# Kernel optimization log

Measured on AMD Instinct MI355X. Metric: run time of the kernel, lower is better.

The kernel has to match this reference:

```python
import jax, jax.numpy as jnp
import numpy as np

MAX_DIST = 32
NUM_HEADS = 16


def setup_inputs() -> dict:
    key = jax.random.key(0)
    ks = jax.random.split(key, 10)
    D = 1024
    B, S = 2, 2048
    hd = D // NUM_HEADS
    sc = 0.02
    return {
        "x": jax.random.normal(ks[0], (B, S, D), dtype=jnp.float32),
        "Wq": jax.random.normal(ks[1], (D, D), dtype=jnp.float32) * sc,
        "bq": jax.random.normal(ks[2], (D,), dtype=jnp.float32) * sc,
        "Wk": jax.random.normal(ks[3], (D, D), dtype=jnp.float32) * sc,
        "bk": jax.random.normal(ks[4], (D,), dtype=jnp.float32) * sc,
        "Wv": jax.random.normal(ks[5], (D, D), dtype=jnp.float32) * sc,
        "bv": jax.random.normal(ks[6], (D,), dtype=jnp.float32) * sc,
        "Wo": jax.random.normal(ks[7], (D, D), dtype=jnp.float32) * sc,
        "bo": jax.random.normal(ks[8], (D,), dtype=jnp.float32) * sc,
        "rel_emb": jax.random.normal(ks[9], (2 * MAX_DIST + 1, hd), dtype=jnp.float32) * sc,
    }


def reference(x, Wq, bq, Wk, bk, Wv, bv, Wo, bo, rel_emb):
    B, S, D = x.shape
    H = NUM_HEADS
    hd = D // H
    scale = hd ** -0.5

    def proj(W, b):
        # [B,S,D] -> [B,H,S,hd]
        return (x @ W + b).reshape(B, S, H, hd).transpose(0, 2, 1, 3)

    q = proj(Wq, bq)
    k = proj(Wk, bk)
    v = proj(Wv, bv)

    # relative position embedding lookup: [S,S,hd]
    pos = jnp.arange(S)
    rel = jnp.clip(pos[:, None] - pos[None, :], -MAX_DIST, MAX_DIST) + MAX_DIST
    rpe = rel_emb[rel]  # [S,S,hd]

    cc = jnp.einsum('bhqd,bhkd->bhqk', q, k) * scale
    cp = jnp.einsum('bhqd,qkd->bhqk', q, rpe) * scale
    attn = jax.nn.softmax(cc + cp, axis=-1)
    ctx = jnp.einsum('bhqk,bhkd->bhqd', attn, v)  # [B,H,S,hd]
    ctx = ctx.transpose(0, 2, 1, 3).reshape(B, S, D)
    return ctx @ Wo + bo
```

## Files before the change

kernel.cpp:

```cpp
#include <hip/hip_runtime.h>

typedef __attribute__((ext_vector_type(4))) float f32x4;
typedef __attribute__((ext_vector_type(8))) short bf16x8;

#define SEQ    2048
#define HD     64
#define NBH    32
#define MTOK   4096
#define DMODEL 1024
#define QBLK   128

__device__ __forceinline__ unsigned short f2b(float f) {
  unsigned int u = __float_as_uint(f);
  u += 0x7fffu + ((u >> 16) & 1u);
  return (unsigned short)(u >> 16);
}
__device__ __forceinline__ float b2f(unsigned short s) {
  return __uint_as_float(((unsigned int)s) << 16);
}
__device__ __forceinline__ unsigned int cvtpk_bf16(float lo, float hi) {
  unsigned int r;
  asm("v_cvt_pk_bf16_f32 %0, %1, %2" : "=v"(r) : "v"(lo), "v"(hi));
  return r;
}
__device__ __forceinline__ void gload16(const void* g, void* l) {
  __builtin_amdgcn_global_load_lds(
      (const __attribute__((address_space(1))) unsigned int*)g,
      (__attribute__((address_space(3))) unsigned int*)l, 16, 0, 0);
}

__global__ __launch_bounds__(256) void k_convert_x(const float* __restrict__ x,
                                                   unsigned short* __restrict__ xb) {
  int i = blockIdx.x * 256 + threadIdx.x;
  float4 v = ((const float4*)x)[i];
  ushort4 o;
  o.x = f2b(v.x); o.y = f2b(v.y); o.z = f2b(v.z); o.w = f2b(v.w);
  ((ushort4*)xb)[i] = o;
}

__global__ __launch_bounds__(256) void k_wtrans(const float* __restrict__ W,
                                                unsigned short* __restrict__ Wt) {
  __shared__ float tile[64 * 65];
  int bi = blockIdx.x, bj = blockIdx.y, t = threadIdx.x;
  for (int p = 0; p < 16; p++) {
    int e = p * 256 + t;
    int r = e >> 6, c = e & 63;
    tile[r * 65 + c] = W[(size_t)(bi * 64 + r) * DMODEL + bj * 64 + c];
  }
  __syncthreads();
  for (int p = 0; p < 16; p++) {
    int e = p * 256 + t;
    int n = e >> 6, k = e & 63;
    Wt[(size_t)(bj * 64 + n) * DMODEL + bi * 64 + k] = f2b(tile[k * 65 + n]);
  }
}

template <int MODE>
__global__ __launch_bounds__(256) void k_gemm_bt(
    const unsigned short* __restrict__ A, const unsigned short* __restrict__ Bt,
    int M, int N, int K,
    const float* __restrict__ bias0, const float* __restrict__ bias1,
    const float* __restrict__ bias2,
    float* __restrict__ Cf,
    unsigned short* __restrict__ Qo, unsigned short* __restrict__ Ko,
    unsigned short* __restrict__ Vo) {
  __shared__ unsigned short As[128 * 64];
  __shared__ unsigned short Bs[128 * 64];
  int bm = blockIdx.x, bn = blockIdx.y;
  int tid = threadIdx.x;
  int w = tid >> 6, lane = tid & 63;
  int lg = lane >> 4, lc = lane & 15;
  int wm = (w >> 1) * 64, wn = (w & 1) * 64;
  f32x4 acc[4][4];
  for (int a = 0; a < 4; a++)
    for (int b = 0; b < 4; b++) acc[a][b] = (f32x4){0.f, 0.f, 0.f, 0.f};
  const unsigned short* ag = A + (size_t)(bm * 128) * K;
  const unsigned short* bg = Bt + (size_t)(bn * 128) * K;
  for (int k0 = 0; k0 < K; k0 += 64) {
    __syncthreads();
    for (int p = 0; p < 4; p++) {
      int c = (w * 4 + p) * 64 + lane;
      int r = c >> 3, ch = (c & 7) ^ (r & 7);
      gload16(ag + (size_t)r * K + k0 + ch * 8, &As[c * 8]);
      gload16(bg + (size_t)r * K + k0 + ch * 8, &Bs[c * 8]);
    }
    __syncthreads();
    for (int kk = 0; kk < 2; kk++) {
      bf16x8 av[4], bv[4];
      for (int mi = 0; mi < 4; mi++) {
        int row = wm + mi * 16 + lc;
        av[mi] = *(const bf16x8*)&As[row * 64 + ((kk * 32 + lg * 8) ^ ((row & 7) << 3))];
      }
      for (int ni = 0; ni < 4; ni++) {
        int row = wn + ni * 16 + lc;
        bv[ni] = *(const bf16x8*)&Bs[row * 64 + ((kk * 32 + lg * 8) ^ ((row & 7) << 3))];
      }
      for (int mi = 0; mi < 4; mi++)
        for (int ni = 0; ni < 4; ni++)
          acc[mi][ni] = __builtin_amdgcn_mfma_f32_16x16x32_bf16(av[mi], bv[ni], acc[mi][ni], 0, 0, 0);
    }
  }
  for (int mi = 0; mi < 4; mi++) {
    for (int i = 0; i < 4; i++) {
      int row = bm * 128 + wm + mi * 16 + 4 * lg + i;
      for (int ni = 0; ni < 4; ni++) {
        int col = bn * 128 + wn + ni * 16 + lc;
        float v = acc[mi][ni][i];
        if (MODE == 0) {
          Cf[(size_t)row * N + col] = v + bias0[col];
        } else {
          int which = col >> 10, hcol = col & 1023;
          const float* bb = which == 0 ? bias0 : (which == 1 ? bias1 : bias2);
          unsigned short* dst = which == 0 ? Qo : (which == 1 ? Ko : Vo);
          int b = row >> 11, s = row & 2047;
          int h = hcol >> 6, d = hcol & 63;
          dst[(((size_t)(b * 16 + h)) * SEQ + s) * HD + d] = f2b(v + bb[hcol]);
        }
      }
    }
  }
}

__global__ __launch_bounds__(256) void k_transpose_v(const unsigned short* __restrict__ V,
                                                     unsigned short* __restrict__ Vt) {
  __shared__ unsigned short tile[64 * 72];
  int sc = blockIdx.x, bh = blockIdx.y, t = threadIdx.x;
  int s0 = sc * 64;
  for (int p = 0; p < 16; p++) {
    int e = p * 256 + t;
    int r = e >> 6, c = e & 63;
    tile[r * 72 + c] = V[(((size_t)bh) * SEQ + s0 + r) * HD + c];
  }
  __syncthreads();
  for (int p = 0; p < 16; p++) {
    int e = p * 256 + t;
    int d = e >> 6, j = e & 63;
    Vt[(((size_t)bh) * HD + d) * SEQ + s0 + j] = tile[j * 72 + d];
  }
}

__global__ __launch_bounds__(256) void k_qr(const unsigned short* __restrict__ Qb,
                                            const float* __restrict__ rel_emb,
                                            float* __restrict__ qr) {
  __shared__ float relS[65 * 66];
  __shared__ unsigned short qS[32 * 64];
  int sc = blockIdx.x, bh = blockIdx.y, t = threadIdx.x;
  int s0 = sc * 32;
  for (int i = t; i < 65 * 64; i += 256) relS[(i >> 6) * 66 + (i & 63)] = rel_emb[i];
  for (int i = t; i < 32 * 64; i += 256) qS[i] = Qb[((size_t)bh * SEQ + s0) * HD + i];
  __syncthreads();
  for (int e = t; e < 32 * 65; e += 256) {
    int sl = e / 65, r = e % 65;
    float acc = 0.f;
    for (int d = 0; d < 64; d++) acc += b2f(qS[sl * 64 + d]) * relS[r * 66 + d];
    qr[((size_t)bh * SEQ + s0 + sl) * 65 + r] = acc;
  }
}

#define C1 0.180336880f
#define C2 11.5415603f
__global__ __launch_bounds__(512, 4) void k_attn(const unsigned short* __restrict__ Qb,
                                                 const unsigned short* __restrict__ Kb,
                                                 const unsigned short* __restrict__ Vtb,
                                                 const float* __restrict__ qr,
                                                 unsigned short* __restrict__ ctx) {
  __shared__ unsigned short Ks[64 * 64];
  __shared__ unsigned short Vts[64 * 64];
  __shared__ unsigned short Ps[8][16 * 64];
  __shared__ float qrs[QBLK * 65];
  int qt = blockIdx.x, bh = blockIdx.y;
  int tid = threadIdx.x, w = tid >> 6, lane = tid & 63;
  int lg = lane >> 4, lc = lane & 15;
  int q0 = qt * QBLK, qw = q0 + w * 16;

  {
    const float* src = qr + ((size_t)bh * SEQ + q0) * 65;
    for (int i = tid; i < QBLK * 65; i += 512) qrs[i] = src[i];
  }
  bf16x8 aq[2];
  {
    const unsigned short* qp = Qb + ((size_t)bh * SEQ + qw + lc) * HD + lg * 8;
    aq[0] = *(const bf16x8*)qp;
    aq[1] = *(const bf16x8*)(qp + 32);
  }
  f32x4 o[4];
  float l[4];
  for (int n = 0; n < 4; n++) o[n] = (f32x4){0.f, 0.f, 0.f, 0.f};
  for (int i = 0; i < 4; i++) l[i] = 0.f;
  __syncthreads();

  float blo[4], bhi[4];
  for (int i = 0; i < 4; i++) {
    int rl = w * 16 + 4 * lg + i;
    blo[i] = fmaf(qrs[rl * 65],      C1, -C2);
    bhi[i] = fmaf(qrs[rl * 65 + 64], C1, -C2);
  }

  for (int kt = 0; kt < SEQ / 64; kt++) {
    int k0 = kt * 64;
    const unsigned short* kg = Kb + ((size_t)bh * SEQ + k0) * HD;
    const unsigned short* vg = Vtb + ((size_t)bh * HD) * SEQ + k0;
    {
      int c = tid;
      int r = c >> 3, ch = (c & 7) ^ (r & 7);
      gload16(kg + (size_t)r * HD + ch * 8, &Ks[c * 8]);
      gload16(vg + (size_t)r * SEQ + ch * 8, &Vts[c * 8]);
    }
    __syncthreads();

    f32x4 s[4];
    #pragma unroll
    for (int n = 0; n < 4; n++) s[n] = (f32x4){0.f, 0.f, 0.f, 0.f};
    #pragma unroll
    for (int n = 0; n < 4; n++) {
      int row = n * 16 + lc;
      #pragma unroll
      for (int kk = 0; kk < 2; kk++) {
        bf16x8 bk = *(const bf16x8*)&Ks[row * 64 + ((kk * 32 + lg * 8) ^ ((row & 7) << 3))];
        s[n] = __builtin_amdgcn_mfma_f32_16x16x32_bf16(aq[kk], bk, s[n], 0, 0, 0);
      }
    }

    int dw = qw - k0;
    bool gather = (dw >= -32) && (dw <= 80);
    #pragma unroll
    for (int n = 0; n < 4; n++)
      #pragma unroll
      for (int i = 0; i < 4; i++) {
        float bf;
        if (gather) {
          int rl = w * 16 + 4 * lg + i;
          int rel = rl + q0 - k0 - n * 16 - lc;
          rel = rel < -32 ? -32 : (rel > 32 ? 32 : rel);
          bf = fmaf(qrs[rl * 65 + rel + 32], C1, -C2);
        } else {
          bf = (dw < 0) ? blo[i] : bhi[i];
        }
        float p = __builtin_amdgcn_exp2f(fmaf(s[n][i], C1, bf));
        s[n][i] = p;
        l[i] += p;
      }

    #pragma unroll
    for (int n = 0; n < 4; n++)
      #pragma unroll
      for (int i = 0; i < 4; i += 2) {
        unsigned int u = cvtpk_bf16(s[n][i], s[n][i + 1]);
        int r0 = 4 * lg + i, r1 = r0 + 1;
        Ps[w][r0 * 64 + ((n * 16 + lc) ^ ((r0 & 7) << 3))] = (unsigned short)u;
        Ps[w][r1 * 64 + ((n * 16 + lc) ^ ((r1 & 7) << 3))] = (unsigned short)(u >> 16);
      }

    #pragma unroll
    for (int kk = 0; kk < 2; kk++) {
      bf16x8 ap = *(const bf16x8*)&Ps[w][lc * 64 + ((kk * 32 + lg * 8) ^ ((lc & 7) << 3))];
      #pragma unroll
      for (int n = 0; n < 4; n++) {
        int row = n * 16 + lc;
        bf16x8 bv = *(const bf16x8*)&Vts[row * 64 + ((kk * 32 + lg * 8) ^ ((row & 7) << 3))];
        o[n] = __builtin_amdgcn_mfma_f32_16x16x32_bf16(ap, bv, o[n], 0, 0, 0);
      }
    }
    __syncthreads();
  }

  int b = bh >> 4, h = bh & 15;
  for (int i = 0; i < 4; i++) {
    float t = l[i];
    t += __shfl_xor(t, 1);
    t += __shfl_xor(t, 2);
    t += __shfl_xor(t, 4);
    t += __shfl_xor(t, 8);
    float inv = 1.f / t;
    int row = qw + 4 * lg + i;
    size_t base = ((size_t)(b * SEQ + row)) * DMODEL + h * HD;
    for (int n = 0; n < 4; n++) ctx[base + n * 16 + lc] = f2b(o[n][i] * inv);
  }
}

extern "C" void kernel_launch(void* const* d_in, const int* in_sizes, int n_in,
                              void* d_out, int out_size, void* d_ws, size_t ws_size,
                              hipStream_t stream) {
  const float* x   = (const float*)d_in[0];
  const float* Wq  = (const float*)d_in[1];
  const float* bq  = (const float*)d_in[2];
  const float* Wk  = (const float*)d_in[3];
  const float* bk  = (const float*)d_in[4];
  const float* Wv  = (const float*)d_in[5];
  const float* bv  = (const float*)d_in[6];
  const float* Wo  = (const float*)d_in[7];
  const float* bo  = (const float*)d_in[8];
  const float* rel = (const float*)d_in[9];
  float* out = (float*)d_out;

  char* ws = (char*)d_ws;
  size_t off = 0;
  auto carve = [&](size_t bytes) -> void* {
    void* p = ws + off;
    off += (bytes + 255) & ~(size_t)255;
    return p;
  };
  unsigned short* xb   = (unsigned short*)carve((size_t)MTOK * DMODEL * 2);
  unsigned short* Wqkv = (unsigned short*)carve((size_t)3 * DMODEL * DMODEL * 2);
  unsigned short* Wot  = (unsigned short*)carve((size_t)DMODEL * DMODEL * 2);
  unsigned short* Qb   = (unsigned short*)carve((size_t)NBH * SEQ * HD * 2);
  unsigned short* Kb   = (unsigned short*)carve((size_t)NBH * SEQ * HD * 2);
  unsigned short* Vb   = (unsigned short*)carve((size_t)NBH * SEQ * HD * 2);
  unsigned short* Vtb  = (unsigned short*)carve((size_t)NBH * SEQ * HD * 2);
  float*          qr   = (float*)carve((size_t)NBH * SEQ * 65 * 4);
  unsigned short* ctx  = (unsigned short*)carve((size_t)MTOK * DMODEL * 2);

  k_convert_x<<<MTOK * DMODEL / 4 / 256, 256, 0, stream>>>(x, xb);
  k_wtrans<<<dim3(16, 16), 256, 0, stream>>>(Wq, Wqkv);
  k_wtrans<<<dim3(16, 16), 256, 0, stream>>>(Wk, Wqkv + (size_t)DMODEL * DMODEL);
  k_wtrans<<<dim3(16, 16), 256, 0, stream>>>(Wv, Wqkv + (size_t)2 * DMODEL * DMODEL);
  k_wtrans<<<dim3(16, 16), 256, 0, stream>>>(Wo, Wot);
  k_gemm_bt<1><<<dim3(32, 24), 256, 0, stream>>>(xb, Wqkv, MTOK, 3 * DMODEL, DMODEL,
                                                 bq, bk, bv, nullptr, Qb, Kb, Vb);
  k_transpose_v<<<dim3(32, 32), 256, 0, stream>>>(Vb, Vtb);
  k_qr<<<dim3(64, 32), 256, 0, stream>>>(Qb, rel, qr);
  k_attn<<<dim3(SEQ / QBLK, NBH), 512, 0, stream>>>(Qb, Kb, Vtb, qr, ctx);
  k_gemm_bt<0><<<dim3(32, 8), 256, 0, stream>>>(ctx, Wot, MTOK, DMODEL, DMODEL,
                                                bo, nullptr, nullptr, out,
                                                nullptr, nullptr, nullptr);
}
```

Baseline: 184.1 us.

## Merge small prep kernels, reorder attention grid, add MFMA priority hints

Folds the four weight-transpose launches into one 3D-grid launch, and merges the V transpose and q·rel_emb kernels into one launch that branches on block index. The attention grid is swapped so consecutive blocks walk across heads rather than query tiles. s_setprio is raised around the MFMA sections of the attention loop. The intent is to cut launch overhead and improve wave scheduling and cache locality, at the cost of divergent block roles in the merged kernel and a higher LDS footprint from its combined shared arrays.

```diff
diff --git a/kernel.cpp b/kernel.cpp
--- a/kernel.cpp
+++ b/kernel.cpp
@@ -38,9 +38,16 @@
   ((ushort4*)xb)[i] = o;
 }
 
-__global__ __launch_bounds__(256) void k_wtrans(const float* __restrict__ W,
-                                                unsigned short* __restrict__ Wt) {
+__global__ __launch_bounds__(256) void k_wtrans_all(const float* __restrict__ Wq,
+                                                    const float* __restrict__ Wk,
+                                                    const float* __restrict__ Wv,
+                                                    const float* __restrict__ Wo,
+                                                    unsigned short* __restrict__ Wqkv,
+                                                    unsigned short* __restrict__ Wot) {
   __shared__ float tile[64 * 65];
+  int z = blockIdx.z;
+  const float* W = (z == 0) ? Wq : (z == 1) ? Wk : (z == 2) ? Wv : Wo;
+  unsigned short* Wt = (z == 3) ? Wot : Wqkv + (size_t)z * DMODEL * DMODEL;
   int bi = blockIdx.x, bj = blockIdx.y, t = threadIdx.x;
   for (int p = 0; p < 16; p++) {
     int e = p * 256 + t;
@@ -121,39 +128,39 @@
   }
 }
 
-__global__ __launch_bounds__(256) void k_transpose_v(const unsigned short* __restrict__ V,
-                                                     unsigned short* __restrict__ Vt) {
+__global__ __launch_bounds__(256) void k_tvqr(const unsigned short* __restrict__ V,
+                                              unsigned short* __restrict__ Vt,
+                                              const unsigned short* __restrict__ Qb,
+                                              const float* __restrict__ rel_emb,
+                                              float* __restrict__ qr) {
   __shared__ unsigned short tile[64 * 72];
-  int sc = blockIdx.x, bh = blockIdx.y, t = threadIdx.x;
-  int s0 = sc * 64;
-  for (int p = 0; p < 16; p++) {
-    int e = p * 256 + t;
-    int r = e >> 6, c = e & 63;
-    tile[r * 72 + c] = V[(((size_t)bh) * SEQ + s0 + r) * HD + c];
-  }
-  __syncthreads();
-  for (int p = 0; p < 16; p++) {
-    int e = p * 256 + t;
-    int d = e >> 6, j = e & 63;
-    Vt[(((size_t)bh) * HD + d) * SEQ + s0 + j] = tile[j * 72 + d];
-  }
-}
-
-__global__ __launch_bounds__(256) void k_qr(const unsigned short* __restrict__ Qb,
-                                            const float* __restrict__ rel_emb,
-                                            float* __restrict__ qr) {
   __shared__ float relS[65 * 66];
   __shared__ unsigned short qS[32 * 64];
-  int sc = blockIdx.x, bh = blockIdx.y, t = threadIdx.x;
-  int s0 = sc * 32;
-  for (int i = t; i < 65 * 64; i += 256) relS[(i >> 6) * 66 + (i & 63)] = rel_emb[i];
-  for (int i = t; i < 32 * 64; i += 256) qS[i] = Qb[((size_t)bh * SEQ + s0) * HD + i];
-  __syncthreads();
-  for (int e = t; e < 32 * 65; e += 256) {
-    int sl = e / 65, r = e % 65;
-    float acc = 0.f;
-    for (int d = 0; d < 64; d++) acc += b2f(qS[sl * 64 + d]) * relS[r * 66 + d];
-    qr[((size_t)bh * SEQ + s0 + sl) * 65 + r] = acc;
+  int bh = blockIdx.y, t = threadIdx.x;
+  if (blockIdx.x < 32) {
+    int s0 = blockIdx.x * 64;
+    for (int p = 0; p < 16; p++) {
+      int e = p * 256 + t;
+      int r = e >> 6, c = e & 63;
+      tile[r * 72 + c] = V[(((size_t)bh) * SEQ + s0 + r) * HD + c];
+    }
+    __syncthreads();
+    for (int p = 0; p < 16; p++) {
+      int e = p * 256 + t;
+      int d = e >> 6, j = e & 63;
+      Vt[(((size_t)bh) * HD + d) * SEQ + s0 + j] = tile[j * 72 + d];
+    }
+  } else {
+    int s0 = (blockIdx.x - 32) * 32;
+    for (int i = t; i < 65 * 64; i += 256) relS[(i >> 6) * 66 + (i & 63)] = rel_emb[i];
+    for (int i = t; i < 32 * 64; i += 256) qS[i] = Qb[((size_t)bh * SEQ + s0) * HD + i];
+    __syncthreads();
+    for (int e = t; e < 32 * 65; e += 256) {
+      int sl = e / 65, r = e % 65;
+      float acc = 0.f;
+      for (int d = 0; d < 64; d++) acc += b2f(qS[sl * 64 + d]) * relS[r * 66 + d];
+      qr[((size_t)bh * SEQ + s0 + sl) * 65 + r] = acc;
+    }
   }
 }
 
@@ -168,7 +175,7 @@
   __shared__ unsigned short Vts[64 * 64];
   __shared__ unsigned short Ps[8][16 * 64];
   __shared__ float qrs[QBLK * 65];
-  int qt = blockIdx.x, bh = blockIdx.y;
+  int bh = blockIdx.x, qt = blockIdx.y;
   int tid = threadIdx.x, w = tid >> 6, lane = tid & 63;
   int lg = lane >> 4, lc = lane & 15;
   int q0 = qt * QBLK, qw = q0 + w * 16;
@@ -211,6 +218,7 @@
     f32x4 s[4];
     #pragma unroll
     for (int n = 0; n < 4; n++) s[n] = (f32x4){0.f, 0.f, 0.f, 0.f};
+    __builtin_amdgcn_s_setprio(1);
     #pragma unroll
     for (int n = 0; n < 4; n++) {
       int row = n * 16 + lc;
@@ -220,6 +228,7 @@
         s[n] = __builtin_amdgcn_mfma_f32_16x16x32_bf16(aq[kk], bk, s[n], 0, 0, 0);
       }
     }
+    __builtin_amdgcn_s_setprio(0);
 
     int dw = qw - k0;
     bool gather = (dw >= -32) && (dw <= 80);
@@ -251,6 +260,7 @@
         Ps[w][r1 * 64 + ((n * 16 + lc) ^ ((r1 & 7) << 3))] = (unsigned short)(u >> 16);
       }
 
+    __builtin_amdgcn_s_setprio(1);
     #pragma unroll
     for (int kk = 0; kk < 2; kk++) {
       bf16x8 ap = *(const bf16x8*)&Ps[w][lc * 64 + ((kk * 32 + lg * 8) ^ ((lc & 7) << 3))];
@@ -261,6 +271,7 @@
         o[n] = __builtin_amdgcn_mfma_f32_16x16x32_bf16(ap, bv, o[n], 0, 0, 0);
       }
     }
+    __builtin_amdgcn_s_setprio(0);
     __syncthreads();
   }
 
@@ -311,15 +322,11 @@
   unsigned short* ctx  = (unsigned short*)carve((size_t)MTOK * DMODEL * 2);
 
   k_convert_x<<<MTOK * DMODEL / 4 / 256, 256, 0, stream>>>(x, xb);
-  k_wtrans<<<dim3(16, 16), 256, 0, stream>>>(Wq, Wqkv);
-  k_wtrans<<<dim3(16, 16), 256, 0, stream>>>(Wk, Wqkv + (size_t)DMODEL * DMODEL);
-  k_wtrans<<<dim3(16, 16), 256, 0, stream>>>(Wv, Wqkv + (size_t)2 * DMODEL * DMODEL);
-  k_wtrans<<<dim3(16, 16), 256, 0, stream>>>(Wo, Wot);
+  k_wtrans_all<<<dim3(16, 16, 4), 256, 0, stream>>>(Wq, Wk, Wv, Wo, Wqkv, Wot);
   k_gemm_bt<1><<<dim3(32, 24), 256, 0, stream>>>(xb, Wqkv, MTOK, 3 * DMODEL, DMODEL,
                                                  bq, bk, bv, nullptr, Qb, Kb, Vb);
-  k_transpose_v<<<dim3(32, 32), 256, 0, stream>>>(Vb, Vtb);
-  k_qr<<<dim3(64, 32), 256, 0, stream>>>(Qb, rel, qr);
-  k_attn<<<dim3(SEQ / QBLK, NBH), 512, 0, stream>>>(Qb, Kb, Vtb, qr, ctx);
+  k_tvqr<<<dim3(96, 32), 256, 0, stream>>>(Vb, Vtb, Qb, rel, qr);
+  k_attn<<<dim3(NBH, SEQ / QBLK), 512, 0, stream>>>(Qb, Kb, Vtb, qr, ctx);
   k_gemm_bt<0><<<dim3(32, 8), 256, 0, stream>>>(ctx, Wot, MTOK, DMODEL, DMODEL,
                                                 bo, nullptr, nullptr, out,
                                                 nullptr, nullptr, nullptr);
```

Measured after the change: 175.0 us. 5.0% less time.
